# Kernel optimization log

Hardware: AMD Instinct MI355X
Metric: run time of the kernel (lower is better)

Reference implementation:

```python
import jax, jax.numpy as jnp
import numpy as np

EMBED_DIM = 1024
N_HEADS = 16
HEAD_DIM = EMBED_DIM // N_HEADS
N_TOKENS = 65536


def setup_inputs() -> dict:
    key = jax.random.key(0)
    ks = jax.random.split(key, 5)
    scale = 1.0 / np.sqrt(EMBED_DIM)
    return {
        "x": jax.random.normal(ks[0], (N_TOKENS, EMBED_DIM), dtype=jnp.float32),
        "Wq": jax.random.normal(ks[1], (EMBED_DIM, EMBED_DIM), dtype=jnp.float32) * scale,
        "Wk": jax.random.normal(ks[2], (EMBED_DIM, EMBED_DIM), dtype=jnp.float32) * scale,
        "Wv": jax.random.normal(ks[3], (EMBED_DIM, EMBED_DIM), dtype=jnp.float32) * scale,
        "Wo": jax.random.normal(ks[4], (EMBED_DIM, EMBED_DIM), dtype=jnp.float32) * scale,
    }


def reference(x, Wq, Wk, Wv, Wo):
    # Linear layers (torch nn.Linear: y = x @ W^T, bias=False)
    q = x @ Wq.T  # [N, E]
    k = x @ Wk.T
    v = x @ Wv.T
    n = x.shape[0]
    q = q.reshape(n, N_HEADS, HEAD_DIM)  # [N, H, D]
    k = k.reshape(n, N_HEADS, HEAD_DIM)
    v = v.reshape(n, N_HEADS, HEAD_DIM)
    # Faithful to original: attention across the HEAD axis per token -> [N, H, H]
    scores = jnp.einsum("nhd,ngd->nhg", q, k) / jnp.sqrt(jnp.asarray(HEAD_DIM, x.dtype))
    attn = jax.nn.softmax(scores, axis=-1)  # [N, H, H]
    out = jnp.einsum("nhg,ngd->nhd", attn, v).reshape(n, EMBED_DIM)
    return out @ Wo.T
```

## Files before the change

### kernel.cpp

```cpp
#include <hip/hip_runtime.h>
#include <hip/hip_bf16.h>
#include <cstdint>

#define DEV static __device__ __forceinline__

typedef __attribute__((ext_vector_type(8))) __bf16 bf16x8;
typedef __attribute__((ext_vector_type(4))) float f32x4;
typedef __attribute__((ext_vector_type(8))) unsigned short ushort8;

constexpr int NTOK = 65536;
constexpr int E = 1024;

DEV unsigned short f2b(float f) {
  unsigned int u = __builtin_bit_cast(unsigned int, f);
  u += 0x7fffu + ((u >> 16) & 1u);
  return (unsigned short)(u >> 16);
}

DEV f32x4 mfma16(bf16x8 a, bf16x8 b, f32x4 c) {
  return __builtin_amdgcn_mfma_f32_16x16x32_bf16(a, b, c, 0, 0, 0);
}

DEV void gload16(const void* g, const void* l) {
  __builtin_amdgcn_global_load_lds(
      (const __attribute__((address_space(1))) void*)g,
      (__attribute__((address_space(3))) void*)l, 16, 0, 0);
}

DEV void BAR() {
  asm volatile("" ::: "memory");
  __builtin_amdgcn_s_barrier();
  asm volatile("" ::: "memory");
  __builtin_amdgcn_sched_barrier(0);
}

#define WAITVM(n_) do { \
  asm volatile("s_waitcnt vmcnt(" #n_ ")" ::: "memory"); \
  __builtin_amdgcn_sched_barrier(0); \
} while (0)

__global__ void cvt8(const float* __restrict__ in, unsigned short* __restrict__ out,
                     int n8) {
  int i = blockIdx.x * blockDim.x + threadIdx.x;
  if (i >= n8) return;
  const float4* p = (const float4*)(in + (size_t)i * 8);
  float4 a = p[0], b = p[1];
  ushort8 r;
  r[0] = f2b(a.x); r[1] = f2b(a.y); r[2] = f2b(a.z); r[3] = f2b(a.w);
  r[4] = f2b(b.x); r[5] = f2b(b.y); r[6] = f2b(b.z); r[7] = f2b(b.w);
  *(ushort8*)(out + (size_t)i * 8) = r;
}

__global__ void cvtW(const float* __restrict__ Wq, const float* __restrict__ Wk,
                     const float* __restrict__ Wv, const float* __restrict__ Wo,
                     unsigned short* __restrict__ out) {
  int i = blockIdx.x * blockDim.x + threadIdx.x;
  int wsel = i >> 17;
  const float* src = wsel == 0 ? Wq : wsel == 1 ? Wk : wsel == 2 ? Wv : Wo;
  int j = i & 131071;
  const float4* p = (const float4*)(src + (size_t)j * 8);
  float4 a = p[0], b = p[1];
  ushort8 r;
  r[0] = f2b(a.x); r[1] = f2b(a.y); r[2] = f2b(a.z); r[3] = f2b(a.w);
  r[4] = f2b(b.x); r[5] = f2b(b.y); r[6] = f2b(b.z); r[7] = f2b(b.w);
  *(ushort8*)(out + (size_t)i * 8) = r;
}

template <typename OutT>
__global__ __launch_bounds__(512, 2) void gemm8(
    const unsigned short* __restrict__ A, const unsigned short* __restrict__ B,
    OutT* __restrict__ C, int M, int N, int K, int nbx) {
  __shared__ char smem[131072];
  char* sA = smem;
  char* sB = smem + 65536;

  const int NT = K >> 6;
  const int nwg = gridDim.x;
  const int cpx = nwg >> 3;
  const int wg = ((int)blockIdx.x & 7) * cpx + ((int)blockIdx.x >> 3);
  const int tm = (wg / nbx) * 256;
  const int tn = (wg % nbx) * 256;

  const int t = threadIdx.x;
  const int w = t >> 6, l = t & 63;
  const int wr = w >> 2, wc = w & 3;
  const int lr = l & 15, q = l >> 4;

  const int srow = w * 8 + (l >> 3);
  const int scol = ((l & 7) ^ (l >> 3)) * 8;
  const int xorv = (lr & 7) << 4;
  const int offk0 = (q * 16) ^ xorv;
  const int offk1 = (64 + q * 16) ^ xorv;
  const int aRB = wr * 8192 + lr * 128;
  const int bRB = wc * 4096 + lr * 128;

#define STAGE_A(tt_, h_) do { \
    const unsigned short* g_ = A + (size_t)(tm + (h_)*128 + srow) * K + (tt_)*64 + scol; \
    const char* d_ = sA + (((tt_) & 1) * 32768 + (h_)*16384 + w * 1024); \
    gload16(g_, d_); \
    gload16(g_ + (size_t)64 * K, d_ + 8192); \
  } while (0)

#define STAGE_B(tt_, h_) do { \
    const unsigned short* g_ = B + (size_t)(tn + (h_)*128 + srow) * K + (tt_)*64 + scol; \
    const char* d_ = sB + (((tt_) & 1) * 32768 + (h_)*16384 + w * 1024); \
    gload16(g_, d_); \
    gload16(g_ + (size_t)64 * K, d_ + 8192); \
  } while (0)

  f32x4 acc[8][4] = {};
  bf16x8 af[4][2];
  bf16x8 bf_[2][2][2];

#define LDA(buf_, mh_) do { \
    _Pragma("unroll") for (int m_ = 0; m_ < 4; ++m_) { \
      af[m_][0] = *(const bf16x8*)(sA + (buf_)*32768 + (mh_)*16384 + m_*2048 + aRB + offk0); \
      af[m_][1] = *(const bf16x8*)(sA + (buf_)*32768 + (mh_)*16384 + m_*2048 + aRB + offk1); \
    } \
  } while (0)

#define LDB(buf_, nh_) do { \
    _Pragma("unroll") for (int n_ = 0; n_ < 2; ++n_) { \
      bf_[nh_][n_][0] = *(const bf16x8*)(sB + (buf_)*32768 + (nh_)*16384 + n_*2048 + bRB + offk0); \
      bf_[nh_][n_][1] = *(const bf16x8*)(sB + (buf_)*32768 + (nh_)*16384 + n_*2048 + bRB + offk1); \
    } \
  } while (0)

#define MM(mh_, nh_) do { \
    __builtin_amdgcn_s_setprio(1); \
    _Pragma("unroll") for (int m_ = 0; m_ < 4; ++m_) \
      _Pragma("unroll") for (int n_ = 0; n_ < 2; ++n_) { \
        acc[(mh_)*4 + m_][(nh_)*2 + n_] = \
            mfma16(af[m_][0], bf_[nh_][n_][0], acc[(mh_)*4 + m_][(nh_)*2 + n_]); \
        acc[(mh_)*4 + m_][(nh_)*2 + n_] = \
            mfma16(af[m_][1], bf_[nh_][n_][1], acc[(mh_)*4 + m_][(nh_)*2 + n_]); \
      } \
    __builtin_amdgcn_s_setprio(0); \
  } while (0)

  STAGE_A(0, 0); STAGE_B(0, 0); STAGE_B(0, 1); STAGE_A(0, 1);
  STAGE_A(1, 0); STAGE_B(1, 0); STAGE_B(1, 1);
  WAITVM(6);
  BAR();

  int T = 0;
  for (; T + 3 < NT; T += 2) {
    LDA(0, 0); LDB(0, 0);
    STAGE_A(T + 1, 1);
    BAR(); MM(0, 0); BAR();
    LDB(0, 1);
    STAGE_A(T + 2, 0);
    BAR(); MM(0, 1); BAR();
    LDA(0, 1);
    STAGE_B(T + 2, 0);
    BAR(); MM(1, 0); BAR();
    STAGE_B(T + 2, 1);
    WAITVM(6);
    BAR(); MM(1, 1); BAR();
    LDA(1, 0); LDB(1, 0);
    STAGE_A(T + 2, 1);
    BAR(); MM(0, 0); BAR();
    LDB(1, 1);
    STAGE_A(T + 3, 0);
    BAR(); MM(0, 1); BAR();
    LDA(1, 1);
    STAGE_B(T + 3, 0);
    BAR(); MM(1, 0); BAR();
    STAGE_B(T + 3, 1);
    WAITVM(6);
    BAR(); MM(1, 1); BAR();
  }
  {
    LDA(0, 0); LDB(0, 0);
    STAGE_A(T + 1, 1);
    BAR(); MM(0, 0); BAR();
    LDB(0, 1);
    BAR(); MM(0, 1); BAR();
    LDA(0, 1);
    BAR(); MM(1, 0); BAR();
    WAITVM(0);
    BAR(); MM(1, 1); BAR();
    LDA(1, 0); LDB(1, 0);
    BAR(); MM(0, 0); BAR();
    LDB(1, 1);
    BAR(); MM(0, 1); BAR();
    LDA(1, 1);
    BAR(); MM(1, 0); BAR();
    BAR(); MM(1, 1); BAR();
  }

#pragma unroll
  for (int mh = 0; mh < 2; ++mh)
#pragma unroll
    for (int m = 0; m < 4; ++m)
#pragma unroll
      for (int nh = 0; nh < 2; ++nh)
#pragma unroll
        for (int n = 0; n < 2; ++n)
#pragma unroll
          for (int j = 0; j < 4; ++j) {
            int row = tm + mh * 128 + wr * 64 + m * 16 + q * 4 + j;
            int col = tn + nh * 128 + wc * 32 + n * 16 + lr;
            float v = acc[mh * 4 + m][nh * 2 + n][j];
            if constexpr (sizeof(OutT) == 2)
              C[(size_t)row * N + col] = (OutT)f2b(v);
            else
              C[(size_t)row * N + col] = v;
          }
#undef STAGE_A
#undef STAGE_B
#undef LDA
#undef LDB
#undef MM
}

__global__ __launch_bounds__(256, 4) void attn16(
    const unsigned short* __restrict__ qkv, unsigned short* __restrict__ out) {
  const int t = threadIdx.x, w = t >> 6, l = t & 63;
  const int tok = blockIdx.x * 4 + w;
  const unsigned short* q = qkv + (size_t)tok * 3072;
  const unsigned short* kp = q + 1024;
  const unsigned short* vp = q + 2048;
  const int lr = l & 15, lk = (l >> 4) * 8;

  bf16x8 aq0 = *reinterpret_cast<const bf16x8*>(q + lr * 64 + lk);
  bf16x8 aq1 = *reinterpret_cast<const bf16x8*>(q + lr * 64 + 32 + lk);
  bf16x8 bk0 = *reinterpret_cast<const bf16x8*>(kp + lr * 64 + lk);
  bf16x8 bk1 = *reinterpret_cast<const bf16x8*>(kp + lr * 64 + 32 + lk);
  f32x4 s = {};
  s = mfma16(bk0, aq0, s);
  s = mfma16(bk1, aq1, s);

  const float cexp = 0.125f * 1.44269504f;
  float mx = fmaxf(fmaxf(s[0], s[1]), fmaxf(s[2], s[3]));
  mx = fmaxf(mx, __shfl_xor(mx, 16));
  mx = fmaxf(mx, __shfl_xor(mx, 32));
  float e0 = exp2f((s[0] - mx) * cexp);
  float e1 = exp2f((s[1] - mx) * cexp);
  float e2 = exp2f((s[2] - mx) * cexp);
  float e3 = exp2f((s[3] - mx) * cexp);
  float sm = (e0 + e1) + (e2 + e3);
  sm += __shfl_xor(sm, 16);
  sm += __shfl_xor(sm, 32);
  float inv = 1.0f / sm;
  float p[4] = {e0 * inv, e1 * inv, e2 * inv, e3 * inv};

  ushort8 au;
#pragma unroll
  for (int jj = 0; jj < 8; ++jj) {
    int src = (lr + (l >> 4) * 32 + (jj >> 2) * 16) & 63;
    float v = __shfl(p[jj & 3], src);
    au[jj] = (l < 32) ? f2b(v) : (unsigned short)0;
  }
  bf16x8 ap = __builtin_bit_cast(bf16x8, au);

  ushort8 zz = {0, 0, 0, 0, 0, 0, 0, 0};
  bf16x8 bv[4];
#pragma unroll
  for (int b = 0; b < 4; ++b) bv[b] = __builtin_bit_cast(bf16x8, zz);
  if (l < 32) {
#pragma unroll
    for (int b = 0; b < 4; ++b) {
      ushort8 tmp;
#pragma unroll
      for (int j = 0; j < 8; ++j) tmp[j] = vp[(lk + j) * 64 + b * 16 + lr];
      bv[b] = __builtin_bit_cast(bf16x8, tmp);
    }
  }

  f32x4 o[4] = {};
#pragma unroll
  for (int b = 0; b < 4; ++b) o[b] = mfma16(ap, bv[b], o[b]);

  unsigned short* op = out + (size_t)tok * 1024;
#pragma unroll
  for (int b = 0; b < 4; ++b)
#pragma unroll
    for (int j = 0; j < 4; ++j)
      op[((l >> 4) * 4 + j) * 64 + b * 16 + lr] = f2b(o[b][j]);
}

extern "C" void kernel_launch(void* const* d_in, const int* in_sizes, int n_in,
                              void* d_out, int out_size, void* d_ws, size_t ws_size,
                              hipStream_t stream) {
  const float* x = (const float*)d_in[0];
  const float* Wq = (const float*)d_in[1];
  const float* Wk = (const float*)d_in[2];
  const float* Wv = (const float*)d_in[3];
  const float* Wo = (const float*)d_in[4];

  unsigned short* xb = (unsigned short*)d_ws;
  unsigned short* wqkv = xb + (size_t)NTOK * E;
  unsigned short* wo = wqkv + (size_t)3 * E * E;
  unsigned short* qkv = wo + (size_t)E * E;
  unsigned short* att = qkv + (size_t)NTOK * 3 * E;

  cvt8<<<(NTOK * E / 8) / 256, 256, 0, stream>>>(x, xb, NTOK * E / 8);
  cvtW<<<(4 * E * E / 8) / 256, 256, 0, stream>>>(Wq, Wk, Wv, Wo, wqkv);

  gemm8<unsigned short><<<(NTOK / 256) * (3 * E / 256), 512, 0, stream>>>(
      xb, wqkv, qkv, NTOK, 3 * E, E, 3 * E / 256);

  attn16<<<NTOK / 4, 256, 0, stream>>>(qkv, att);

  gemm8<float><<<(NTOK / 256) * (E / 256), 512, 0, stream>>>(
      att, wo, (float*)d_out, NTOK, E, E, E / 256);
}
```

Baseline: 740.5 us.

## Shrink GEMM tile to 256x128 with K-step 32 for higher occupancy

The GEMM block tile shrinks from 256x256 with a K-step of 64 to 256x128 with a K-step of 32. Shared memory drops from 128KB to 48KB and launch bounds rise to 4 blocks per CU, with the LDS swizzle and staging addressing rewritten to match. The aim is more resident waves to hide latency and more blocks for better load balance. The cost is lower arithmetic intensity per tile, more global traffic for the A operand, and twice as many barrier-heavy iterations.

```diff
diff --git a/kernel.cpp b/kernel.cpp
--- a/kernel.cpp
+++ b/kernel.cpp
@@ -67,80 +67,66 @@
 }
 
 template <typename OutT>
-__global__ __launch_bounds__(512, 2) void gemm8(
+__global__ __launch_bounds__(512, 4) void gemm8(
     const unsigned short* __restrict__ A, const unsigned short* __restrict__ B,
     OutT* __restrict__ C, int M, int N, int K, int nbx) {
-  __shared__ char smem[131072];
+  __shared__ char smem[49152];
   char* sA = smem;
-  char* sB = smem + 65536;
-
-  const int NT = K >> 6;
+  char* sB = smem + 32768;
+
+  const int NT = K >> 5;
   const int nwg = gridDim.x;
   const int cpx = nwg >> 3;
   const int wg = ((int)blockIdx.x & 7) * cpx + ((int)blockIdx.x >> 3);
   const int tm = (wg / nbx) * 256;
-  const int tn = (wg % nbx) * 256;
+  const int tn = (wg % nbx) * 128;
 
   const int t = threadIdx.x;
   const int w = t >> 6, l = t & 63;
   const int wr = w >> 2, wc = w & 3;
   const int lr = l & 15, q = l >> 4;
 
-  const int srow = w * 8 + (l >> 3);
-  const int scol = ((l & 7) ^ (l >> 3)) * 8;
-  const int xorv = (lr & 7) << 4;
-  const int offk0 = (q * 16) ^ xorv;
-  const int offk1 = (64 + q * 16) ^ xorv;
-  const int aRB = wr * 8192 + lr * 128;
-  const int bRB = wc * 4096 + lr * 128;
+  const int srow = w * 16 + (l >> 2);
+  const int scol = ((l & 3) ^ ((l >> 3) & 3)) * 8;
+  const int offk = (q ^ ((lr >> 1) & 3)) * 16;
+  const int aRB = (wr * 64 + lr) * 64;
+  const int bRB = (wc * 16 + lr) * 64;
 
 #define STAGE_A(tt_, h_) do { \
-    const unsigned short* g_ = A + (size_t)(tm + (h_)*128 + srow) * K + (tt_)*64 + scol; \
-    const char* d_ = sA + (((tt_) & 1) * 32768 + (h_)*16384 + w * 1024); \
+    const unsigned short* g_ = A + (size_t)(tm + (h_)*128 + srow) * K + (tt_)*32 + scol; \
+    const char* d_ = sA + (((tt_) & 1) * 16384 + (h_)*8192 + w * 1024); \
     gload16(g_, d_); \
-    gload16(g_ + (size_t)64 * K, d_ + 8192); \
-  } while (0)
-
-#define STAGE_B(tt_, h_) do { \
-    const unsigned short* g_ = B + (size_t)(tn + (h_)*128 + srow) * K + (tt_)*64 + scol; \
-    const char* d_ = sB + (((tt_) & 1) * 32768 + (h_)*16384 + w * 1024); \
+  } while (0)
+
+#define STAGE_B(tt_) do { \
+    const unsigned short* g_ = B + (size_t)(tn + srow) * K + (tt_)*32 + scol; \
+    const char* d_ = sB + (((tt_) & 1) * 8192 + w * 1024); \
     gload16(g_, d_); \
-    gload16(g_ + (size_t)64 * K, d_ + 8192); \
-  } while (0)
-
-  f32x4 acc[8][4] = {};
-  bf16x8 af[4][2];
-  bf16x8 bf_[2][2][2];
+  } while (0)
+
+  f32x4 acc[8][2] = {};
+  bf16x8 af[4];
+  bf16x8 bf_[2];
 
 #define LDA(buf_, mh_) do { \
-    _Pragma("unroll") for (int m_ = 0; m_ < 4; ++m_) { \
-      af[m_][0] = *(const bf16x8*)(sA + (buf_)*32768 + (mh_)*16384 + m_*2048 + aRB + offk0); \
-      af[m_][1] = *(const bf16x8*)(sA + (buf_)*32768 + (mh_)*16384 + m_*2048 + aRB + offk1); \
-    } \
+    _Pragma("unroll") for (int m_ = 0; m_ < 4; ++m_) \
+      af[m_] = *(const bf16x8*)(sA + (buf_)*16384 + (mh_)*8192 + aRB + m_*1024 + offk); \
   } while (0)
 
 #define LDB(buf_, nh_) do { \
-    _Pragma("unroll") for (int n_ = 0; n_ < 2; ++n_) { \
-      bf_[nh_][n_][0] = *(const bf16x8*)(sB + (buf_)*32768 + (nh_)*16384 + n_*2048 + bRB + offk0); \
-      bf_[nh_][n_][1] = *(const bf16x8*)(sB + (buf_)*32768 + (nh_)*16384 + n_*2048 + bRB + offk1); \
-    } \
+    bf_[nh_] = *(const bf16x8*)(sB + (buf_)*8192 + (nh_)*4096 + bRB + offk); \
   } while (0)
 
 #define MM(mh_, nh_) do { \
     __builtin_amdgcn_s_setprio(1); \
     _Pragma("unroll") for (int m_ = 0; m_ < 4; ++m_) \
-      _Pragma("unroll") for (int n_ = 0; n_ < 2; ++n_) { \
-        acc[(mh_)*4 + m_][(nh_)*2 + n_] = \
-            mfma16(af[m_][0], bf_[nh_][n_][0], acc[(mh_)*4 + m_][(nh_)*2 + n_]); \
-        acc[(mh_)*4 + m_][(nh_)*2 + n_] = \
-            mfma16(af[m_][1], bf_[nh_][n_][1], acc[(mh_)*4 + m_][(nh_)*2 + n_]); \
-      } \
+      acc[(mh_)*4 + m_][nh_] = mfma16(af[m_], bf_[nh_], acc[(mh_)*4 + m_][nh_]); \
     __builtin_amdgcn_s_setprio(0); \
   } while (0)
 
-  STAGE_A(0, 0); STAGE_B(0, 0); STAGE_B(0, 1); STAGE_A(0, 1);
-  STAGE_A(1, 0); STAGE_B(1, 0); STAGE_B(1, 1);
-  WAITVM(6);
+  STAGE_A(0, 0); STAGE_A(0, 1); STAGE_B(0);
+  STAGE_A(1, 0); STAGE_B(1);
+  WAITVM(2);
   BAR();
 
   int T = 0;
@@ -152,10 +138,9 @@
     STAGE_A(T + 2, 0);
     BAR(); MM(0, 1); BAR();
     LDA(0, 1);
-    STAGE_B(T + 2, 0);
-    BAR(); MM(1, 0); BAR();
-    STAGE_B(T + 2, 1);
-    WAITVM(6);
+    STAGE_B(T + 2);
+    BAR(); MM(1, 0); BAR();
+    WAITVM(2);
     BAR(); MM(1, 1); BAR();
     LDA(1, 0); LDB(1, 0);
     STAGE_A(T + 2, 1);
@@ -164,10 +149,9 @@
     STAGE_A(T + 3, 0);
     BAR(); MM(0, 1); BAR();
     LDA(1, 1);
-    STAGE_B(T + 3, 0);
-    BAR(); MM(1, 0); BAR();
-    STAGE_B(T + 3, 1);
-    WAITVM(6);
+    STAGE_B(T + 3);
+    BAR(); MM(1, 0); BAR();
+    WAITVM(2);
     BAR(); MM(1, 1); BAR();
   }
   {
@@ -196,17 +180,15 @@
 #pragma unroll
       for (int nh = 0; nh < 2; ++nh)
 #pragma unroll
-        for (int n = 0; n < 2; ++n)
-#pragma unroll
-          for (int j = 0; j < 4; ++j) {
-            int row = tm + mh * 128 + wr * 64 + m * 16 + q * 4 + j;
-            int col = tn + nh * 128 + wc * 32 + n * 16 + lr;
-            float v = acc[mh * 4 + m][nh * 2 + n][j];
-            if constexpr (sizeof(OutT) == 2)
-              C[(size_t)row * N + col] = (OutT)f2b(v);
-            else
-              C[(size_t)row * N + col] = v;
-          }
+        for (int j = 0; j < 4; ++j) {
+          int row = tm + mh * 128 + wr * 64 + m * 16 + q * 4 + j;
+          int col = tn + nh * 64 + wc * 16 + lr;
+          float v = acc[mh * 4 + m][nh][j];
+          if constexpr (sizeof(OutT) == 2)
+            C[(size_t)row * N + col] = (OutT)f2b(v);
+          else
+            C[(size_t)row * N + col] = v;
+        }
 #undef STAGE_A
 #undef STAGE_B
 #undef LDA
@@ -298,11 +280,11 @@
   cvt8<<<(NTOK * E / 8) / 256, 256, 0, stream>>>(x, xb, NTOK * E / 8);
   cvtW<<<(4 * E * E / 8) / 256, 256, 0, stream>>>(Wq, Wk, Wv, Wo, wqkv);
 
-  gemm8<unsigned short><<<(NTOK / 256) * (3 * E / 256), 512, 0, stream>>>(
-      xb, wqkv, qkv, NTOK, 3 * E, E, 3 * E / 256);
+  gemm8<unsigned short><<<(NTOK / 256) * (3 * E / 128), 512, 0, stream>>>(
+      xb, wqkv, qkv, NTOK, 3 * E, E, 3 * E / 128);
 
   attn16<<<NTOK / 4, 256, 0, stream>>>(qkv, att);
 
-  gemm8<float><<<(NTOK / 256) * (E / 256), 512, 0, stream>>>(
-      att, wo, (float*)d_out, NTOK, E, E, E / 256);
-}
+  gemm8<float><<<(NTOK / 256) * (E / 128), 512, 0, stream>>>(
+      att, wo, (float*)d_out, NTOK, E, E, E / 128);
+}
```

Measured after the change: 854.5 us. +15.4%, slower.

## Merge GEMM main-loop phases into four larger MFMA blocks per iteration

Applied to the files above, without the earlier changes.

Restructures the software-pipelined GEMM main loop from eight barrier-separated MFMA phases per two K-tiles into four, each running two MM quadrants back to back. Global-to-LDS staging is regrouped so one A tile and two B tiles are issued together, and vmcnt waits are raised and placed before every phase. The aim is fewer workgroup barriers and longer uninterrupted MFMA bursts, at the cost of coarser interleaving of loads with compute and more fragment registers live at once. Correctness depends on the new vmcnt thresholds covering all outstanding loads into the buffers being read.

```diff
diff --git a/kernel.cpp b/kernel.cpp
--- a/kernel.cpp
+++ b/kernel.cpp
@@ -140,53 +140,41 @@
 
   STAGE_A(0, 0); STAGE_B(0, 0); STAGE_B(0, 1); STAGE_A(0, 1);
   STAGE_A(1, 0); STAGE_B(1, 0); STAGE_B(1, 1);
-  WAITVM(6);
+  WAITVM(8);
   BAR();
 
   int T = 0;
   for (; T + 3 < NT; T += 2) {
-    LDA(0, 0); LDB(0, 0);
+    LDA(0, 0); LDB(0, 0); LDB(0, 1);
     STAGE_A(T + 1, 1);
-    BAR(); MM(0, 0); BAR();
-    LDB(0, 1);
-    STAGE_A(T + 2, 0);
-    BAR(); MM(0, 1); BAR();
+    WAITVM(8);
+    BAR(); MM(0, 0); MM(0, 1); BAR();
     LDA(0, 1);
-    STAGE_B(T + 2, 0);
-    BAR(); MM(1, 0); BAR();
-    STAGE_B(T + 2, 1);
-    WAITVM(6);
-    BAR(); MM(1, 1); BAR();
-    LDA(1, 0); LDB(1, 0);
+    STAGE_A(T + 2, 0); STAGE_B(T + 2, 0); STAGE_B(T + 2, 1);
+    WAITVM(8);
+    BAR(); MM(1, 0); MM(1, 1); BAR();
+    LDA(1, 0); LDB(1, 0); LDB(1, 1);
     STAGE_A(T + 2, 1);
-    BAR(); MM(0, 0); BAR();
-    LDB(1, 1);
-    STAGE_A(T + 3, 0);
-    BAR(); MM(0, 1); BAR();
+    WAITVM(8);
+    BAR(); MM(0, 0); MM(0, 1); BAR();
     LDA(1, 1);
-    STAGE_B(T + 3, 0);
-    BAR(); MM(1, 0); BAR();
-    STAGE_B(T + 3, 1);
-    WAITVM(6);
-    BAR(); MM(1, 1); BAR();
+    STAGE_A(T + 3, 0); STAGE_B(T + 3, 0); STAGE_B(T + 3, 1);
+    WAITVM(8);
+    BAR(); MM(1, 0); MM(1, 1); BAR();
   }
   {
-    LDA(0, 0); LDB(0, 0);
+    LDA(0, 0); LDB(0, 0); LDB(0, 1);
     STAGE_A(T + 1, 1);
-    BAR(); MM(0, 0); BAR();
-    LDB(0, 1);
-    BAR(); MM(0, 1); BAR();
+    WAITVM(8);
+    BAR(); MM(0, 0); MM(0, 1); BAR();
     LDA(0, 1);
-    BAR(); MM(1, 0); BAR();
+    WAITVM(2);
+    BAR(); MM(1, 0); MM(1, 1); BAR();
+    LDA(1, 0); LDB(1, 0); LDB(1, 1);
     WAITVM(0);
-    BAR(); MM(1, 1); BAR();
-    LDA(1, 0); LDB(1, 0);
-    BAR(); MM(0, 0); BAR();
-    LDB(1, 1);
-    BAR(); MM(0, 1); BAR();
+    BAR(); MM(0, 0); MM(0, 1); BAR();
     LDA(1, 1);
-    BAR(); MM(1, 0); BAR();
-    BAR(); MM(1, 1); BAR();
+    BAR(); MM(1, 0); MM(1, 1); BAR();
   }
 
 #pragma unroll
```

After: 756.7 us. +2.2%, slower.
